# Kernel tuning notes

Hardware: AMD Instinct MI355X
Metric: run time of the kernel (lower is better)

## Reference

```python
import jax, jax.numpy as jnp
import numpy as np
import math

B, T, C = 2, 2048, 1024
N_HEADS = 16  # config.head_size in the original (actually number of heads)
HEAD_DIM = C // N_HEADS


def setup_inputs() -> dict:
    key = jax.random.key(0)
    k1, k2, k3 = jax.random.split(key, 3)
    s = 1.0 / math.sqrt(C)
    return {
        "x": jax.random.normal(k1, (B, T, C), dtype=jnp.float32),
        "W_attn": jax.random.normal(k2, (C, 3 * C), dtype=jnp.float32) * s,
        "b_attn": jnp.zeros((3 * C,), dtype=jnp.float32),
        "W_proj": jax.random.normal(k3, (C, C), dtype=jnp.float32) * s,
        "b_proj": jnp.zeros((C,), dtype=jnp.float32),
    }


def reference(x, W_attn, b_attn, W_proj, b_proj):
    Bsz, Tlen, Cdim = x.shape
    qkv = x @ W_attn + b_attn                      # [B,T,3C]
    q, k, v = jnp.split(qkv, 3, axis=-1)
    # [B,T,C] -> [B,H,T,D]
    def to_heads(t):
        return t.reshape(Bsz, Tlen, N_HEADS, HEAD_DIM).transpose(0, 2, 1, 3)
    q, k, v = to_heads(q), to_heads(k), to_heads(v)
    # NOTE: original multiplies by sqrt(head_dim) (faithful to source, not 1/sqrt)
    scale = jnp.asarray(math.sqrt(HEAD_DIM), dtype=x.dtype)
    att = jnp.einsum("bhqd,bhkd->bhqk", q, k) * scale
    causal = jnp.tril(jnp.ones((Tlen, Tlen), dtype=bool))
    att = jnp.where(causal[None, None, :, :], att, jnp.asarray(-jnp.inf, x.dtype))
    att = jax.nn.softmax(att, axis=-1)
    # dropout layers are identity in eval mode
    y = jnp.einsum("bhqk,bhkd->bhqd", att, v)
    y = y.transpose(0, 2, 1, 3).reshape(Bsz, Tlen, Cdim)
    return y @ W_proj + b_proj
```

## Files before the change

kernel.cpp:

```cpp
#include <hip/hip_runtime.h>
#include <hip/hip_bf16.h>


#define B_  2
#define T_  2048
#define C_  1024
#define H_  16
#define D_  64
#define M_  (B_ * T_)
#define N3_ (3 * C_)

typedef __attribute__((ext_vector_type(8))) short s16x8;
typedef __attribute__((ext_vector_type(4))) short s16x4;
typedef __attribute__((ext_vector_type(4))) float f32x4;

typedef const __attribute__((address_space(1))) unsigned int gu32_t;
typedef __attribute__((address_space(3))) unsigned int lu32_t;

__device__ __forceinline__ void gload_lds16(const short* g, short* l) {
    __builtin_amdgcn_global_load_lds((gu32_t*)g, (lu32_t*)l, 16, 0, 0);
}

__device__ __forceinline__ float b2f(unsigned short u) {
    return __uint_as_float(((unsigned)u) << 16);
}
__device__ __forceinline__ unsigned short f2b(float f) {
    unsigned u = __float_as_uint(f);
    return (unsigned short)((u + 0x7FFFu + ((u >> 16) & 1u)) >> 16);
}

__global__ __launch_bounds__(256) void cvt_split(
    const float* __restrict__ in, short* __restrict__ oh, short* __restrict__ ol, int n)
{
    int i = (blockIdx.x * 256 + threadIdx.x) * 8;
    if (i >= n) return;
    float4 a = *(const float4*)&in[i];
    float4 b = *(const float4*)&in[i + 4];
    float v[8] = {a.x, a.y, a.z, a.w, b.x, b.y, b.z, b.w};
    s16x8 h, l;
    #pragma unroll
    for (int j = 0; j < 8; j++) {
        unsigned short hb = f2b(v[j]);
        h[j] = (short)hb;
        l[j] = (short)f2b(v[j] - b2f(hb));
    }
    *(s16x8*)&oh[i] = h;
    *(s16x8*)&ol[i] = l;
}

__global__ __launch_bounds__(256) void cvtT_split(
    const float* __restrict__ in, short* __restrict__ oh, short* __restrict__ ol,
    int R, int Cn)
{
    __shared__ short th[64][80];
    __shared__ short tl[64][80];
    const int tid = threadIdx.x;
    const int k0 = blockIdx.y * 64;
    const int n0 = blockIdx.x * 64;
    {
        int rl = tid >> 4, cl = (tid & 15) * 4;
        #pragma unroll
        for (int i = 0; i < 4; i++) {
            int kr = rl + i * 16;
            float4 v4 = *(const float4*)&in[(size_t)(k0 + kr) * Cn + n0 + cl];
            float v[4] = {v4.x, v4.y, v4.z, v4.w};
            #pragma unroll
            for (int j = 0; j < 4; j++) {
                unsigned short hb = f2b(v[j]);
                th[cl + j][kr] = (short)hb;
                tl[cl + j][kr] = (short)f2b(v[j] - b2f(hb));
            }
        }
    }
    __syncthreads();
    {
        int ro = tid >> 2, co = (tid & 3) * 16;
        *(s16x8*)&oh[(size_t)(n0 + ro) * R + k0 + co]     = *(s16x8*)&th[ro][co];
        *(s16x8*)&oh[(size_t)(n0 + ro) * R + k0 + co + 8] = *(s16x8*)&th[ro][co + 8];
        *(s16x8*)&ol[(size_t)(n0 + ro) * R + k0 + co]     = *(s16x8*)&tl[ro][co];
        *(s16x8*)&ol[(size_t)(n0 + ro) * R + k0 + co + 8] = *(s16x8*)&tl[ro][co + 8];
    }
}

__global__ __launch_bounds__(256) void cvtT_bf16(
    const float* __restrict__ in, short* __restrict__ out, int R, int Cn)
{
    __shared__ short t[64][80];
    const int tid = threadIdx.x;
    const int k0 = blockIdx.y * 64;
    const int n0 = blockIdx.x * 64;
    {
        int rl = tid >> 4, cl = (tid & 15) * 4;
        #pragma unroll
        for (int i = 0; i < 4; i++) {
            int kr = rl + i * 16;
            float4 v = *(const float4*)&in[(size_t)(k0 + kr) * Cn + n0 + cl];
            t[cl + 0][kr] = (short)f2b(v.x);
            t[cl + 1][kr] = (short)f2b(v.y);
            t[cl + 2][kr] = (short)f2b(v.z);
            t[cl + 3][kr] = (short)f2b(v.w);
        }
    }
    __syncthreads();
    {
        int ro = tid >> 2, co = (tid & 3) * 16;
        *(s16x8*)&out[(size_t)(n0 + ro) * R + k0 + co]     = *(s16x8*)&t[ro][co];
        *(s16x8*)&out[(size_t)(n0 + ro) * R + k0 + co + 8] = *(s16x8*)&t[ro][co + 8];
    }
}

__global__ __launch_bounds__(256) void qkv_qk(
    const short* __restrict__ Ah, const short* __restrict__ Al,
    const short* __restrict__ BTh, const short* __restrict__ BTl,
    const float* __restrict__ bias,
    short* __restrict__ Qh, short* __restrict__ Ql,
    short* __restrict__ Kh, short* __restrict__ Kl)
{
    __shared__ short Ash[128 * 32], Asl[128 * 32];
    __shared__ short Bsh[128 * 32], Bsl[128 * 32];

    const int tid  = threadIdx.x;
    const int wave = tid >> 6, lane = tid & 63;
    const int wm = wave >> 1, wn = wave & 1;
    const int lm = lane & 15, lq = lane >> 4;
    const int m0 = blockIdx.y * 128, n0 = blockIdx.x * 128;
    const int gr = (lane >> 2);
    const int gc = (lane & 3) * 8;

    f32x4 acc[4][4] = {};

    for (int k0 = 0; k0 < C_; k0 += 32) {
        __syncthreads();
        #pragma unroll
        for (int j = 0; j < 2; j++) {
            int s = wave * 2 + j;
            int row = s * 16 + gr;
            size_t ga = (size_t)(m0 + row) * C_ + k0 + gc;
            size_t gb = (size_t)(n0 + row) * C_ + k0 + gc;
            gload_lds16(&Ah[ga],  &Ash[s * 512]);
            gload_lds16(&Al[ga],  &Asl[s * 512]);
            gload_lds16(&BTh[gb], &Bsh[s * 512]);
            gload_lds16(&BTl[gb], &Bsl[s * 512]);
        }
        __syncthreads();

        s16x8 ah[4], al[4], bh[4], bl[4];
        #pragma unroll
        for (int mi = 0; mi < 4; mi++) {
            int r = wm * 64 + mi * 16 + lm;
            ah[mi] = *(const s16x8*)&Ash[r * 32 + lq * 8];
            al[mi] = *(const s16x8*)&Asl[r * 32 + lq * 8];
        }
        #pragma unroll
        for (int nj = 0; nj < 4; nj++) {
            int r = wn * 64 + nj * 16 + lm;
            bh[nj] = *(const s16x8*)&Bsh[r * 32 + lq * 8];
            bl[nj] = *(const s16x8*)&Bsl[r * 32 + lq * 8];
        }
        #pragma unroll
        for (int mi = 0; mi < 4; mi++)
            #pragma unroll
            for (int nj = 0; nj < 4; nj++) {
                acc[mi][nj] = __builtin_amdgcn_mfma_f32_16x16x32_bf16(
                    ah[mi], bh[nj], acc[mi][nj], 0, 0, 0);
                acc[mi][nj] = __builtin_amdgcn_mfma_f32_16x16x32_bf16(
                    ah[mi], bl[nj], acc[mi][nj], 0, 0, 0);
                acc[mi][nj] = __builtin_amdgcn_mfma_f32_16x16x32_bf16(
                    al[mi], bh[nj], acc[mi][nj], 0, 0, 0);
            }
    }

    #pragma unroll
    for (int nj = 0; nj < 4; nj++) {
        int n = n0 + wn * 64 + nj * 16 + lm;
        float bv = bias[n];
        int isK = n >> 10;
        int c = n & (C_ - 1);
        int h = c >> 6, d = c & (D_ - 1);
        short* dh = isK ? Kh : Qh;
        short* dl = isK ? Kl : Ql;
        float scale = isK ? 1.0f : 8.0f;
        #pragma unroll
        for (int mi = 0; mi < 4; mi++) {
            #pragma unroll
            for (int r = 0; r < 4; r++) {
                int m  = m0 + wm * 64 + mi * 16 + lq * 4 + r;
                int bb = m >> 11, t = m & (T_ - 1);
                float v = (acc[mi][nj][r] + bv) * scale;
                size_t idx = (((size_t)bb * H_ + h) * T_ + t) * D_ + d;
                unsigned short hb = f2b(v);
                dh[idx] = (short)hb;
                dl[idx] = (short)f2b(v - b2f(hb));
            }
        }
    }
}

__global__ __launch_bounds__(256) void qkv_v(
    const short* __restrict__ Ah, const short* __restrict__ BTh,
    const float* __restrict__ bias, short* __restrict__ VT)
{
    __shared__ short Ash[128 * 32];
    __shared__ short Bsh[128 * 32];

    const int tid  = threadIdx.x;
    const int wave = tid >> 6, lane = tid & 63;
    const int wm = wave >> 1, wn = wave & 1;
    const int lm = lane & 15, lq = lane >> 4;
    const int m0 = blockIdx.y * 128, n0 = blockIdx.x * 128;
    const int gr = (lane >> 2);
    const int gc = (lane & 3) * 8;

    f32x4 acc[4][4] = {};

    for (int k0 = 0; k0 < C_; k0 += 32) {
        __syncthreads();
        #pragma unroll
        for (int j = 0; j < 2; j++) {
            int s = wave * 2 + j;
            int row = s * 16 + gr;
            gload_lds16(&Ah[(size_t)(m0 + row) * C_ + k0 + gc],  &Ash[s * 512]);
            gload_lds16(&BTh[(size_t)(n0 + row) * C_ + k0 + gc], &Bsh[s * 512]);
        }
        __syncthreads();

        s16x8 af[4], bfr[4];
        #pragma unroll
        for (int mi = 0; mi < 4; mi++)
            af[mi] = *(const s16x8*)&Ash[(wm * 64 + mi * 16 + lm) * 32 + lq * 8];
        #pragma unroll
        for (int nj = 0; nj < 4; nj++)
            bfr[nj] = *(const s16x8*)&Bsh[(wn * 64 + nj * 16 + lm) * 32 + lq * 8];
        #pragma unroll
        for (int mi = 0; mi < 4; mi++)
            #pragma unroll
            for (int nj = 0; nj < 4; nj++)
                acc[mi][nj] = __builtin_amdgcn_mfma_f32_16x16x32_bf16(
                    af[mi], bfr[nj], acc[mi][nj], 0, 0, 0);
    }

    #pragma unroll
    for (int nj = 0; nj < 4; nj++) {
        int n = n0 + wn * 64 + nj * 16 + lm;
        float bv = bias[n];
        int h = n >> 6, d = n & (D_ - 1);
        #pragma unroll
        for (int mi = 0; mi < 4; mi++) {
            #pragma unroll
            for (int r = 0; r < 4; r++) {
                int m  = m0 + wm * 64 + mi * 16 + lq * 4 + r;
                int bb = m >> 11, t = m & (T_ - 1);
                VT[(((size_t)bb * H_ + h) * D_ + d) * T_ + t] =
                    (short)f2b(acc[mi][nj][r] + bv);
            }
        }
    }
}

__global__ __launch_bounds__(256) void proj_mfma(
    const short* __restrict__ A, const short* __restrict__ BT,
    const float* __restrict__ bias, float* __restrict__ out)
{
    __shared__ short Ash[128 * 32];
    __shared__ short Bsh[128 * 32];

    const int tid  = threadIdx.x;
    const int wave = tid >> 6, lane = tid & 63;
    const int wm = wave >> 1, wn = wave & 1;
    const int lm = lane & 15, lq = lane >> 4;
    const int m0 = blockIdx.y * 128, n0 = blockIdx.x * 128;
    const int gr = (lane >> 2);
    const int gc = (lane & 3) * 8;

    f32x4 acc[4][4] = {};

    for (int k0 = 0; k0 < C_; k0 += 32) {
        __syncthreads();
        #pragma unroll
        for (int j = 0; j < 2; j++) {
            int s = wave * 2 + j;
            int row = s * 16 + gr;
            gload_lds16(&A[(size_t)(m0 + row) * C_ + k0 + gc],  &Ash[s * 512]);
            gload_lds16(&BT[(size_t)(n0 + row) * C_ + k0 + gc], &Bsh[s * 512]);
        }
        __syncthreads();

        s16x8 af[4], bfr[4];
        #pragma unroll
        for (int mi = 0; mi < 4; mi++)
            af[mi] = *(const s16x8*)&Ash[(wm * 64 + mi * 16 + lm) * 32 + lq * 8];
        #pragma unroll
        for (int nj = 0; nj < 4; nj++)
            bfr[nj] = *(const s16x8*)&Bsh[(wn * 64 + nj * 16 + lm) * 32 + lq * 8];
        #pragma unroll
        for (int mi = 0; mi < 4; mi++)
            #pragma unroll
            for (int nj = 0; nj < 4; nj++)
                acc[mi][nj] = __builtin_amdgcn_mfma_f32_16x16x32_bf16(
                    af[mi], bfr[nj], acc[mi][nj], 0, 0, 0);
    }

    #pragma unroll
    for (int nj = 0; nj < 4; nj++) {
        int n = n0 + wn * 64 + nj * 16 + lm;
        float bv = bias[n];
        #pragma unroll
        for (int mi = 0; mi < 4; mi++) {
            #pragma unroll
            for (int r = 0; r < 4; r++) {
                int m = m0 + wm * 64 + mi * 16 + lq * 4 + r;
                out[(size_t)m * C_ + n] = acc[mi][nj][r] + bv;
            }
        }
    }
}

__global__ __launch_bounds__(256) void attn_mfma(
    const short* __restrict__ Qh, const short* __restrict__ Ql,
    const short* __restrict__ Kh, const short* __restrict__ Kl,
    const short* __restrict__ VT, short* __restrict__ Yb)
{
    __shared__ short Qsh[64][72], Qsl[64][72];
    __shared__ short Ksh[64][72], Ksl[64][72];
    __shared__ short Vt [64][72];
    __shared__ short Ps [4][16][72];

    const int tid  = threadIdx.x;
    const int wave = tid >> 6, lane = tid & 63;
    const int lm   = lane & 15, quad = lane >> 4;

    const int bid = blockIdx.x;
    const int xcd = bid & 7, s = bid >> 3;
    const int bh  = xcd * 4 + (s >> 4);
    const int qx  = s & 15;
    const int b   = bh >> 4, h = bh & (H_ - 1);
    const size_t base  = (size_t)bh * T_ * D_;
    const size_t vbase = (size_t)bh * D_ * T_;

    s16x8 pkh[2], pkl[2], pvt[2];
    const int src = tid >> 3;
    const int sch = (tid & 7) * 8;

    for (int half = 0; half < 2; half++) {
        const int qt = (half == 0) ? qx : 31 - qx;
        const int q0 = qt * 64;

        __syncthreads();
        #pragma unroll
        for (int i = 0; i < 2; i++) {
            int row = i * 32 + src;
            size_t g = base + (size_t)(q0 + row) * D_ + sch;
            *(s16x8*)&Qsh[row][sch] = *(const s16x8*)&Qh[g];
            *(s16x8*)&Qsl[row][sch] = *(const s16x8*)&Ql[g];
        }
        __syncthreads();

        s16x8 bqh[2], bql[2];
        #pragma unroll
        for (int kc = 0; kc < 2; kc++) {
            bqh[kc] = *(const s16x8*)&Qsh[wave * 16 + lm][kc * 32 + quad * 8];
            bql[kc] = *(const s16x8*)&Qsl[wave * 16 + lm][kc * 32 + quad * 8];
        }

        #pragma unroll
        for (int i = 0; i < 2; i++) {
            int row = i * 32 + src;
            size_t g = base + (size_t)(row) * D_ + sch;
            pkh[i] = *(const s16x8*)&Kh[g];
            pkl[i] = *(const s16x8*)&Kl[g];
            pvt[i] = *(const s16x8*)&VT[vbase + (size_t)row * T_ + sch];
        }

        float mrow = -INFINITY, lrow = 0.f;
        f32x4 O[4] = {};

        for (int kt = 0; kt <= qt; kt++) {
            __syncthreads();
            #pragma unroll
            for (int i = 0; i < 2; i++) {
                int row = i * 32 + src;
                *(s16x8*)&Ksh[row][sch] = pkh[i];
                *(s16x8*)&Ksl[row][sch] = pkl[i];
                *(s16x8*)&Vt [row][sch] = pvt[i];
            }
            if (kt < qt) {
                #pragma unroll
                for (int i = 0; i < 2; i++) {
                    int row = i * 32 + src;
                    size_t g = base + (size_t)((kt + 1) * 64 + row) * D_ + sch;
                    pkh[i] = *(const s16x8*)&Kh[g];
                    pkl[i] = *(const s16x8*)&Kl[g];
                    pvt[i] = *(const s16x8*)&VT[vbase + (size_t)row * T_ + (kt + 1) * 64 + sch];
                }
            }
            __syncthreads();

            f32x4 S[4] = {};
            #pragma unroll
            for (int t = 0; t < 4; t++) {
                #pragma unroll
                for (int kc = 0; kc < 2; kc++) {
                    s16x8 kh8 = *(const s16x8*)&Ksh[t * 16 + lm][kc * 32 + quad * 8];
                    s16x8 kl8 = *(const s16x8*)&Ksl[t * 16 + lm][kc * 32 + quad * 8];
                    S[t] = __builtin_amdgcn_mfma_f32_16x16x32_bf16(kh8, bqh[kc], S[t], 0, 0, 0);
                    S[t] = __builtin_amdgcn_mfma_f32_16x16x32_bf16(kl8, bqh[kc], S[t], 0, 0, 0);
                    S[t] = __builtin_amdgcn_mfma_f32_16x16x32_bf16(kh8, bql[kc], S[t], 0, 0, 0);
                }
            }

            const int qg = wave * 16 + lm;
            if (kt == qt) {
                #pragma unroll
                for (int t = 0; t < 4; t++)
                    #pragma unroll
                    for (int r = 0; r < 4; r++)
                        if ((t * 16 + quad * 4 + r) > qg) S[t][r] = -INFINITY;
            }

            float rm = -INFINITY;
            #pragma unroll
            for (int t = 0; t < 4; t++)
                #pragma unroll
                for (int r = 0; r < 4; r++) rm = fmaxf(rm, S[t][r]);
            rm = fmaxf(rm, __shfl_xor(rm, 16, 64));
            rm = fmaxf(rm, __shfl_xor(rm, 32, 64));
            float mnew  = fmaxf(mrow, rm);
            float alpha = __expf(mrow - mnew);
            mrow = mnew;
            float rs = 0.f;
            #pragma unroll
            for (int t = 0; t < 4; t++)
                #pragma unroll
                for (int r = 0; r < 4; r++) {
                    S[t][r] = __expf(S[t][r] - mnew);
                    rs += S[t][r];
                }
            rs += __shfl_xor(rs, 16, 64);
            rs += __shfl_xor(rs, 32, 64);
            lrow = lrow * alpha + rs;

            float al[4];
            #pragma unroll
            for (int r = 0; r < 4; r++) al[r] = __shfl(alpha, quad * 4 + r, 64);
            #pragma unroll
            for (int t = 0; t < 4; t++)
                #pragma unroll
                for (int r = 0; r < 4; r++) O[t][r] *= al[r];

            #pragma unroll
            for (int t = 0; t < 4; t++) {
                s16x4 p;
                #pragma unroll
                for (int r = 0; r < 4; r++)
                    p[r] = (short)(__float_as_uint(S[t][r]) >> 16);
                *(s16x4*)&Ps[wave][lm][t * 16 + quad * 4] = p;
            }

            s16x8 ap[2];
            #pragma unroll
            for (int kc = 0; kc < 2; kc++)
                ap[kc] = *(const s16x8*)&Ps[wave][lm][kc * 32 + quad * 8];
            #pragma unroll
            for (int t = 0; t < 4; t++) {
                #pragma unroll
                for (int kc = 0; kc < 2; kc++) {
                    s16x8 bv = *(const s16x8*)&Vt[t * 16 + lm][kc * 32 + quad * 8];
                    O[t] = __builtin_amdgcn_mfma_f32_16x16x32_bf16(ap[kc], bv, O[t], 0, 0, 0);
                }
            }
        }

        float li[4];
        #pragma unroll
        for (int r = 0; r < 4; r++)
            li[r] = 1.0f / __shfl(lrow, quad * 4 + r, 64);
        #pragma unroll
        for (int t = 0; t < 4; t++)
            #pragma unroll
            for (int r = 0; r < 4; r++) {
                int q = q0 + wave * 16 + quad * 4 + r;
                int d = t * 16 + lm;
                Yb[((size_t)b * T_ + q) * C_ + h * D_ + d] =
                    (short)f2b(O[t][r] * li[r]);
            }
    }
}

extern "C" void kernel_launch(void* const* d_in, const int* in_sizes, int n_in,
                              void* d_out, int out_size, void* d_ws, size_t ws_size,
                              hipStream_t stream)
{
    const float* x      = (const float*)d_in[0];
    const float* W_attn = (const float*)d_in[1];
    const float* b_attn = (const float*)d_in[2];
    const float* W_proj = (const float*)d_in[3];
    const float* b_proj = (const float*)d_in[4];
    float* out = (float*)d_out;

    char* ws = (char*)d_ws;
    const size_t MB = 1024 * 1024;
    short* Qh   = (short*)(ws);
    short* Ql   = (short*)(ws +  8 * MB);
    short* Kh   = (short*)(ws + 16 * MB);
    short* Kl   = (short*)(ws + 24 * MB);
    short* xh   = (short*)(ws + 32 * MB);
    short* xl   = (short*)(ws + 40 * MB);
    short* WaTh = (short*)(ws + 48 * MB);
    short* WaTl = (short*)(ws + 54 * MB);
    short* WpT  = (short*)(ws + 60 * MB);
    short* VT   = (short*)(ws + 40 * MB);
    short* Yb   = (short*)(ws + 32 * MB);

    cvt_split <<<dim3(M_ * C_ / 2048), 256, 0, stream>>>(x, xh, xl, M_ * C_);
    cvtT_split<<<dim3(N3_ / 64, C_ / 64), 256, 0, stream>>>(W_attn, WaTh, WaTl, C_, N3_);
    cvtT_bf16 <<<dim3(C_ / 64, C_ / 64), 256, 0, stream>>>(W_proj, WpT, C_, C_);

    qkv_qk <<<dim3(16, 32), 256, 0, stream>>>(xh, xl, WaTh, WaTl, b_attn,
                                              Qh, Ql, Kh, Kl);
    qkv_v  <<<dim3(8, 32), 256, 0, stream>>>(xh, WaTh + (size_t)2048 * C_,
                                             b_attn + 2048, VT);
    attn_mfma<<<dim3(512), 256, 0, stream>>>(Qh, Ql, Kh, Kl, VT, Yb);
    proj_mfma<<<dim3(8, 32), 256, 0, stream>>>(Yb, WpT, b_proj, out);
}
```

Measured before the change: 255.8 us.

## Split attention into one block per query tile and use exp2 with folded log2e scale

```diff
diff --git a/kernel.cpp b/kernel.cpp
--- a/kernel.cpp
+++ b/kernel.cpp
@@ -27,6 +27,13 @@
 __device__ __forceinline__ unsigned short f2b(float f) {
     unsigned u = __float_as_uint(f);
     return (unsigned short)((u + 0x7FFFu + ((u >> 16) & 1u)) >> 16);
+}
+__device__ __forceinline__ float fexp2(float x) {
+#if __has_builtin(__builtin_amdgcn_exp2f)
+    return __builtin_amdgcn_exp2f(x);
+#else
+    return exp2f(x);
+#endif
 }
 
 __global__ __launch_bounds__(256) void cvt_split(
@@ -179,7 +186,7 @@
         int h = c >> 6, d = c & (D_ - 1);
         short* dh = isK ? Kh : Qh;
         short* dl = isK ? Kl : Ql;
-        float scale = isK ? 1.0f : 8.0f;
+        float scale = isK ? 1.0f : 11.541560327111708f;
         #pragma unroll
         for (int mi = 0; mi < 4; mi++) {
             #pragma unroll
@@ -320,7 +327,6 @@
     const short* __restrict__ Kh, const short* __restrict__ Kl,
     const short* __restrict__ VT, short* __restrict__ Yb)
 {
-    __shared__ short Qsh[64][72], Qsl[64][72];
     __shared__ short Ksh[64][72], Ksl[64][72];
     __shared__ short Vt [64][72];
     __shared__ short Ps [4][16][72];
@@ -330,160 +336,159 @@
     const int lm   = lane & 15, quad = lane >> 4;
 
     const int bid = blockIdx.x;
-    const int xcd = bid & 7, s = bid >> 3;
-    const int bh  = xcd * 4 + (s >> 4);
-    const int qx  = s & 15;
+    const int xcd = bid & 7;
+    const int r_  = bid >> 3;
+    const int bhl = r_ & 3;
+    const int u   = r_ >> 2;
+    const int g_  = u >> 3, j_ = u & 7;
+    const int qt  = (g_ == 0) ? j_ : (g_ == 1) ? 15 - j_
+                  : (g_ == 2) ? 16 + j_ : 31 - j_;
+    const int bh  = xcd * 4 + bhl;
     const int b   = bh >> 4, h = bh & (H_ - 1);
+    const int q0  = qt * 64;
     const size_t base  = (size_t)bh * T_ * D_;
     const size_t vbase = (size_t)bh * D_ * T_;
 
-    s16x8 pkh[2], pkl[2], pvt[2];
     const int src = tid >> 3;
     const int sch = (tid & 7) * 8;
 
-    for (int half = 0; half < 2; half++) {
-        const int qt = (half == 0) ? qx : 31 - qx;
-        const int q0 = qt * 64;
-
+    #pragma unroll
+    for (int i = 0; i < 2; i++) {
+        int row = i * 32 + src;
+        size_t gq = base + (size_t)(q0 + row) * D_ + sch;
+        *(s16x8*)&Ksh[row][sch] = *(const s16x8*)&Qh[gq];
+        *(s16x8*)&Ksl[row][sch] = *(const s16x8*)&Ql[gq];
+    }
+    __syncthreads();
+    s16x8 bqh[2], bql[2];
+    #pragma unroll
+    for (int kc = 0; kc < 2; kc++) {
+        bqh[kc] = *(const s16x8*)&Ksh[wave * 16 + lm][kc * 32 + quad * 8];
+        bql[kc] = *(const s16x8*)&Ksl[wave * 16 + lm][kc * 32 + quad * 8];
+    }
+
+    s16x8 pkh[2], pkl[2], pvt[2];
+    #pragma unroll
+    for (int i = 0; i < 2; i++) {
+        int row = i * 32 + src;
+        size_t gk = base + (size_t)row * D_ + sch;
+        pkh[i] = *(const s16x8*)&Kh[gk];
+        pkl[i] = *(const s16x8*)&Kl[gk];
+        pvt[i] = *(const s16x8*)&VT[vbase + (size_t)row * T_ + sch];
+    }
+
+    float mrow = -INFINITY, lrow = 0.f;
+    f32x4 O[4] = {};
+
+    for (int kt = 0; kt <= qt; kt++) {
         __syncthreads();
         #pragma unroll
         for (int i = 0; i < 2; i++) {
             int row = i * 32 + src;
-            size_t g = base + (size_t)(q0 + row) * D_ + sch;
-            *(s16x8*)&Qsh[row][sch] = *(const s16x8*)&Qh[g];
-            *(s16x8*)&Qsl[row][sch] = *(const s16x8*)&Ql[g];
-        }
-        __syncthreads();
-
-        s16x8 bqh[2], bql[2];
-        #pragma unroll
-        for (int kc = 0; kc < 2; kc++) {
-            bqh[kc] = *(const s16x8*)&Qsh[wave * 16 + lm][kc * 32 + quad * 8];
-            bql[kc] = *(const s16x8*)&Qsl[wave * 16 + lm][kc * 32 + quad * 8];
-        }
-
-        #pragma unroll
-        for (int i = 0; i < 2; i++) {
-            int row = i * 32 + src;
-            size_t g = base + (size_t)(row) * D_ + sch;
-            pkh[i] = *(const s16x8*)&Kh[g];
-            pkl[i] = *(const s16x8*)&Kl[g];
-            pvt[i] = *(const s16x8*)&VT[vbase + (size_t)row * T_ + sch];
-        }
-
-        float mrow = -INFINITY, lrow = 0.f;
-        f32x4 O[4] = {};
-
-        for (int kt = 0; kt <= qt; kt++) {
-            __syncthreads();
+            *(s16x8*)&Ksh[row][sch] = pkh[i];
+            *(s16x8*)&Ksl[row][sch] = pkl[i];
+            *(s16x8*)&Vt [row][sch] = pvt[i];
+        }
+        if (kt < qt) {
             #pragma unroll
             for (int i = 0; i < 2; i++) {
                 int row = i * 32 + src;
-                *(s16x8*)&Ksh[row][sch] = pkh[i];
-                *(s16x8*)&Ksl[row][sch] = pkl[i];
-                *(s16x8*)&Vt [row][sch] = pvt[i];
-            }
-            if (kt < qt) {
-                #pragma unroll
-                for (int i = 0; i < 2; i++) {
-                    int row = i * 32 + src;
-                    size_t g = base + (size_t)((kt + 1) * 64 + row) * D_ + sch;
-                    pkh[i] = *(const s16x8*)&Kh[g];
-                    pkl[i] = *(const s16x8*)&Kl[g];
-                    pvt[i] = *(const s16x8*)&VT[vbase + (size_t)row * T_ + (kt + 1) * 64 + sch];
-                }
-            }
-            __syncthreads();
-
-            f32x4 S[4] = {};
-            #pragma unroll
-            for (int t = 0; t < 4; t++) {
-                #pragma unroll
-                for (int kc = 0; kc < 2; kc++) {
-                    s16x8 kh8 = *(const s16x8*)&Ksh[t * 16 + lm][kc * 32 + quad * 8];
-                    s16x8 kl8 = *(const s16x8*)&Ksl[t * 16 + lm][kc * 32 + quad * 8];
-                    S[t] = __builtin_amdgcn_mfma_f32_16x16x32_bf16(kh8, bqh[kc], S[t], 0, 0, 0);
-                    S[t] = __builtin_amdgcn_mfma_f32_16x16x32_bf16(kl8, bqh[kc], S[t], 0, 0, 0);
-                    S[t] = __builtin_amdgcn_mfma_f32_16x16x32_bf16(kh8, bql[kc], S[t], 0, 0, 0);
-                }
-            }
-
-            const int qg = wave * 16 + lm;
-            if (kt == qt) {
-                #pragma unroll
-                for (int t = 0; t < 4; t++)
-                    #pragma unroll
-                    for (int r = 0; r < 4; r++)
-                        if ((t * 16 + quad * 4 + r) > qg) S[t][r] = -INFINITY;
-            }
-
-            float rm = -INFINITY;
+                size_t gk = base + (size_t)((kt + 1) * 64 + row) * D_ + sch;
+                pkh[i] = *(const s16x8*)&Kh[gk];
+                pkl[i] = *(const s16x8*)&Kl[gk];
+                pvt[i] = *(const s16x8*)&VT[vbase + (size_t)row * T_ + (kt + 1) * 64 + sch];
+            }
+        }
+        __syncthreads();
+
+        f32x4 S[4] = {};
+        #pragma unroll
+        for (int t = 0; t < 4; t++) {
+            #pragma unroll
+            for (int kc = 0; kc < 2; kc++) {
+                s16x8 kh8 = *(const s16x8*)&Ksh[t * 16 + lm][kc * 32 + quad * 8];
+                s16x8 kl8 = *(const s16x8*)&Ksl[t * 16 + lm][kc * 32 + quad * 8];
+                S[t] = __builtin_amdgcn_mfma_f32_16x16x32_bf16(kh8, bqh[kc], S[t], 0, 0, 0);
+                S[t] = __builtin_amdgcn_mfma_f32_16x16x32_bf16(kl8, bqh[kc], S[t], 0, 0, 0);
+                S[t] = __builtin_amdgcn_mfma_f32_16x16x32_bf16(kh8, bql[kc], S[t], 0, 0, 0);
+            }
+        }
+
+        const int qg = wave * 16 + lm;
+        if (kt == qt) {
             #pragma unroll
             for (int t = 0; t < 4; t++)
                 #pragma unroll
-                for (int r = 0; r < 4; r++) rm = fmaxf(rm, S[t][r]);
-            rm = fmaxf(rm, __shfl_xor(rm, 16, 64));
-            rm = fmaxf(rm, __shfl_xor(rm, 32, 64));
-            float mnew  = fmaxf(mrow, rm);
-            float alpha = __expf(mrow - mnew);
-            mrow = mnew;
-            float rs = 0.f;
-            #pragma unroll
-            for (int t = 0; t < 4; t++)
-                #pragma unroll
-                for (int r = 0; r < 4; r++) {
-                    S[t][r] = __expf(S[t][r] - mnew);
-                    rs += S[t][r];
-                }
-            rs += __shfl_xor(rs, 16, 64);
-            rs += __shfl_xor(rs, 32, 64);
-            lrow = lrow * alpha + rs;
-
-            float al[4];
-            #pragma unroll
-            for (int r = 0; r < 4; r++) al[r] = __shfl(alpha, quad * 4 + r, 64);
-            #pragma unroll
-            for (int t = 0; t < 4; t++)
-                #pragma unroll
-                for (int r = 0; r < 4; r++) O[t][r] *= al[r];
-
-            #pragma unroll
-            for (int t = 0; t < 4; t++) {
-                s16x4 p;
-                #pragma unroll
                 for (int r = 0; r < 4; r++)
-                    p[r] = (short)(__float_as_uint(S[t][r]) >> 16);
-                *(s16x4*)&Ps[wave][lm][t * 16 + quad * 4] = p;
-            }
-
-            s16x8 ap[2];
-            #pragma unroll
-            for (int kc = 0; kc < 2; kc++)
-                ap[kc] = *(const s16x8*)&Ps[wave][lm][kc * 32 + quad * 8];
-            #pragma unroll
-            for (int t = 0; t < 4; t++) {
-                #pragma unroll
-                for (int kc = 0; kc < 2; kc++) {
-                    s16x8 bv = *(const s16x8*)&Vt[t * 16 + lm][kc * 32 + quad * 8];
-                    O[t] = __builtin_amdgcn_mfma_f32_16x16x32_bf16(ap[kc], bv, O[t], 0, 0, 0);
-                }
-            }
-        }
-
-        float li[4];
-        #pragma unroll
-        for (int r = 0; r < 4; r++)
-            li[r] = 1.0f / __shfl(lrow, quad * 4 + r, 64);
+                    if ((t * 16 + quad * 4 + r) > qg) S[t][r] = -INFINITY;
+        }
+
+        float rm = -INFINITY;
         #pragma unroll
         for (int t = 0; t < 4; t++)
             #pragma unroll
+            for (int r = 0; r < 4; r++) rm = fmaxf(rm, S[t][r]);
+        rm = fmaxf(rm, __shfl_xor(rm, 16, 64));
+        rm = fmaxf(rm, __shfl_xor(rm, 32, 64));
+        float mnew  = fmaxf(mrow, rm);
+        float alpha = fexp2(mrow - mnew);
+        mrow = mnew;
+        float rs = 0.f;
+        #pragma unroll
+        for (int t = 0; t < 4; t++)
+            #pragma unroll
             for (int r = 0; r < 4; r++) {
-                int q = q0 + wave * 16 + quad * 4 + r;
-                int d = t * 16 + lm;
-                Yb[((size_t)b * T_ + q) * C_ + h * D_ + d] =
-                    (short)f2b(O[t][r] * li[r]);
-            }
-    }
+                S[t][r] = fexp2(S[t][r] - mnew);
+                rs += S[t][r];
+            }
+        rs += __shfl_xor(rs, 16, 64);
+        rs += __shfl_xor(rs, 32, 64);
+        lrow = lrow * alpha + rs;
+
+        float al[4];
+        #pragma unroll
+        for (int r = 0; r < 4; r++) al[r] = __shfl(alpha, quad * 4 + r, 64);
+        #pragma unroll
+        for (int t = 0; t < 4; t++)
+            #pragma unroll
+            for (int r = 0; r < 4; r++) O[t][r] *= al[r];
+
+        #pragma unroll
+        for (int t = 0; t < 4; t++) {
+            s16x4 p;
+            #pragma unroll
+            for (int r = 0; r < 4; r++)
+                p[r] = (short)(__float_as_uint(S[t][r]) >> 16);
+            *(s16x4*)&Ps[wave][lm][t * 16 + quad * 4] = p;
+        }
+
+        s16x8 ap[2];
+        #pragma unroll
+        for (int kc = 0; kc < 2; kc++)
+            ap[kc] = *(const s16x8*)&Ps[wave][lm][kc * 32 + quad * 8];
+        #pragma unroll
+        for (int t = 0; t < 4; t++) {
+            #pragma unroll
+            for (int kc = 0; kc < 2; kc++) {
+                s16x8 bv = *(const s16x8*)&Vt[t * 16 + lm][kc * 32 + quad * 8];
+                O[t] = __builtin_amdgcn_mfma_f32_16x16x32_bf16(ap[kc], bv, O[t], 0, 0, 0);
+            }
+        }
+    }
+
+    float li[4];
+    #pragma unroll
+    for (int r = 0; r < 4; r++)
+        li[r] = 1.0f / __shfl(lrow, quad * 4 + r, 64);
+    #pragma unroll
+    for (int t = 0; t < 4; t++)
+        #pragma unroll
+        for (int r = 0; r < 4; r++) {
+            int q = q0 + wave * 16 + quad * 4 + r;
+            int d = t * 16 + lm;
+            Yb[((size_t)b * T_ + q) * C_ + h * D_ + d] =
+                (short)f2b(O[t][r] * li[r]);
+        }
 }
 
 extern "C" void kernel_launch(void* const* d_in, const int* in_sizes, int n_in,
@@ -519,6 +524,6 @@
                                               Qh, Ql, Kh, Kl);
     qkv_v  <<<dim3(8, 32), 256, 0, stream>>>(xh, WaTh + (size_t)2048 * C_,
                                              b_attn + 2048, VT);
-    attn_mfma<<<dim3(512), 256, 0, stream>>>(Qh, Ql, Kh, Kl, VT, Yb);
+    attn_mfma<<<dim3(1024), 256, 0, stream>>>(Qh, Ql, Kh, Kl, VT, Yb);
     proj_mfma<<<dim3(8, 32), 256, 0, stream>>>(Yb, WpT, b_proj, out);
 }
```

Result: no change. 254.6 us (-0.5%).
